# Kernel optimization log

Measured on AMD Instinct MI355X. Metric: run time of the kernel, lower is better.

## Reference

```python
import jax, jax.numpy as jnp
import numpy as np

N_HEADS = 8; DH = 64; G = 4; K = 9
C = N_HEADS * DH; CG = C // G
FACTOR = 2.0; TAU = 1.0
SCALE = DH ** -0.5


def _conv1x1(x, w, b):
    # x: (C, *spatial), w: (O, C), b: (O,)
    y = jnp.tensordot(w, x, axes=([1], [0]))
    return y + b.reshape((-1,) + (1,) * (y.ndim - 1))


def _dwconv(x, w, b):
    # depthwise 3x3, SAME padding; x (N,Cg,H,W), w (Cg,1,3,3)
    y = jax.lax.conv_general_dilated(x, w, (1, 1), 'SAME',
                                     feature_group_count=x.shape[1],
                                     dimension_numbers=('NCHW', 'OIHW', 'NCHW'))
    return y + b[None, :, None, None]


def _ln(x, g, b):
    # LayerNormProxy: LN over channel dim of NCHW (torch default eps=1e-5)
    m = jnp.mean(x, axis=1, keepdims=True)
    v = jnp.var(x, axis=1, keepdims=True)
    return (x - m) / jnp.sqrt(v + 1e-5) * g[None, :, None, None] + b[None, :, None, None]


def _grid_sample(img, grid):
    # bilinear, align_corners=True, padding_mode='zeros'
    # img (N,C,H,W), grid (N,Hg,Wg,2) with (x,y) in [-1,1]
    N, Cc, H, W = img.shape
    gx = (grid[..., 0] + 1.0) * 0.5 * (W - 1)
    gy = (grid[..., 1] + 1.0) * 0.5 * (H - 1)
    x0 = jnp.floor(gx); y0 = jnp.floor(gy)

    def g(yy, xx):
        yi = jnp.clip(yy, 0, H - 1).astype(jnp.int32)
        xi = jnp.clip(xx, 0, W - 1).astype(jnp.int32)
        ok = ((yy >= 0) & (yy <= H - 1) & (xx >= 0) & (xx <= W - 1)).astype(img.dtype)
        vals = jax.vmap(lambda im, a, b: im[:, a, b])(img, yi, xi)  # (N,C,Hg,Wg)
        return vals * ok[:, None]

    wx1 = gx - x0; wx0 = 1.0 - wx1
    wy1 = gy - y0; wy0 = 1.0 - wy1
    return (g(y0, x0) * (wy0 * wx0)[:, None]
            + g(y0, x0 + 1) * (wy0 * wx1)[:, None]
            + g(y0 + 1, x0) * (wy1 * wx0)[:, None]
            + g(y0 + 1, x0 + 1) * (wy1 * wx1)[:, None])


def _forward(x, idx, labels, wq, bq, wk, bk, wv, bv, wo, bo,
             ow1, ob1, g1, b1, ow2, ob2, g2, b2, ow3):
    _, _, H, W = x.shape
    n = idx.shape[0]
    iy, ix = idx[:, 0], idx[:, 1]

    q = _conv1x1(x[0], wq, bq)[None]               # (1,C,H,W)
    q_off = q.reshape(G, CG, H, W)                 # (b g) c h w with b=1
    q_sel = q[0][:, iy, ix]                        # (C,n)

    # offset predictor: dwconv -> LN -> GELU (x2) -> 1x1 (no bias)
    t = jax.nn.gelu(_ln(_dwconv(q_off, ow1, ob1), g1, b1), approximate=False)
    t = jax.nn.gelu(_ln(_dwconv(t, ow2, ob2), g2, b2), approximate=False)
    offset = jnp.einsum('gchw,oc->gohw', t, ow3)   # (G,2K,H,W)

    # offset_range_factor > 0: tanh * [1/H,1/W] (tiled K times) * factor
    rng = jnp.tile(jnp.array([1.0 / H, 1.0 / W], offset.dtype), K)
    offset = jnp.tanh(offset) * rng[None, :, None, None] * FACTOR
    off = offset.transpose(0, 2, 3, 1).reshape(G, H, W, K, 2)  # (g,h,w,K,(y,x))

    # reference points in [-1,1] (y,x), unfolded over 3x3 window w/ replication pad
    ry = (jnp.arange(H, dtype=x.dtype) + 0.5) / H * 2.0 - 1.0
    rx = (jnp.arange(W, dtype=x.dtype) + 0.5) / W * 2.0 - 1.0
    ref = jnp.stack(jnp.meshgrid(ry, rx, indexing='ij'), 0)    # (2,H,W)
    pad = jnp.pad(ref, ((0, 0), (1, 1), (1, 1)), mode='edge')
    patches = jnp.stack([pad[:, dy:dy + H, dx:dx + W]
                         for dy in range(3) for dx in range(3)], 0)  # (K,2,H,W)
    ref_unf = patches.transpose(2, 3, 0, 1)                    # (H,W,K,2)

    pos = off + ref_unf[None]                                  # (G,H,W,K,2)
    pos = pos.transpose(0, 3, 1, 2, 4).reshape(G * K, H, W, 2)
    grid = pos[..., ::-1]                                      # (x,y) order

    # gather per-group channels at K learned locations per position
    xg = x.reshape(G, CG, H, W)
    img = jnp.broadcast_to(xg[:, None], (G, K, CG, H, W)).reshape(G * K, CG, H, W)
    xs = _grid_sample(img, grid)                               # (GK,CG,H,W)
    xs = xs.reshape(G, K, CG, H, W).transpose(0, 2, 1, 3, 4).reshape(C, K, H, W)
    xs_sel = xs[:, :, iy, ix]                                  # (C,K,n)

    k = _conv1x1(xs_sel, wk, bk).reshape(N_HEADS, DH, K, n).transpose(0, 1, 3, 2)  # (h,d,n,K)
    v = _conv1x1(xs_sel, wv, bv).reshape(N_HEADS, DH, K, n).transpose(0, 1, 3, 2)
    qh = q_sel.reshape(N_HEADS, DH, n)

    attn = jnp.einsum('hdn,hdnk->hnk', qh, k) * SCALE
    attn = jax.nn.softmax(attn / TAU, axis=-1)                 # (h,n,K)
    out = jnp.einsum('hnk,hdnk->hdn', attn, v).reshape(C, n)
    y = _conv1x1(out, wo, bo).T                                # (n, dim_out)

    sig = jax.nn.sigmoid(y[jnp.arange(n), labels])

    # second grid_sample over full channels at the same learned positions
    img_full = jnp.broadcast_to(x, (G * K, C, H, W))
    xr = _grid_sample(img_full, grid)                          # (GK,C,H,W)
    xr_sel = xr[:, :, iy, ix].transpose(2, 0, 1)               # (n,GK,C)
    return y, attn, xr_sel, sig


def setup_inputs() -> dict:
    key = jax.random.key(0)
    ks = jax.random.split(key, 16)
    H = W = 64; n = 2048; s = 0.02
    return dict(
        x=jax.random.normal(ks[0], (1, C, H, W), jnp.float32),
        idx=jax.random.randint(ks[1], (n, 2), 0, H),
        labels=jax.random.randint(ks[2], (n,), 0, C),
        wq=jax.random.normal(ks[3], (C, C), jnp.float32) * s, bq=jnp.zeros((C,), jnp.float32),
        wk=jax.random.normal(ks[4], (C, C), jnp.float32) * s, bk=jnp.zeros((C,), jnp.float32),
        wv=jax.random.normal(ks[5], (C, C), jnp.float32) * s, bv=jnp.zeros((C,), jnp.float32),
        wo=jax.random.normal(ks[6], (C, C), jnp.float32) * s, bo=jnp.zeros((C,), jnp.float32),
        ow1=jax.random.normal(ks[7], (CG, 1, 3, 3), jnp.float32) * s, ob1=jnp.zeros((CG,), jnp.float32),
        g1=jnp.ones((CG,), jnp.float32), b1=jnp.zeros((CG,), jnp.float32),
        ow2=jax.random.normal(ks[8], (CG, 1, 3, 3), jnp.float32) * s, ob2=jnp.zeros((CG,), jnp.float32),
        g2=jnp.ones((CG,), jnp.float32), b2=jnp.zeros((CG,), jnp.float32),
        ow3=jax.random.normal(ks[9], (2 * K, CG), jnp.float32) * s,
    )


def reference(x, idx, labels, wq, bq, wk, bk, wv, bv, wo, bo,
              ow1, ob1, g1, b1, ow2, ob2, g2, b2, ow3):
    return _forward(x, idx, labels, wq, bq, wk, bk, wv, bv, wo, bo,
                    ow1, ob1, g1, b1, ow2, ob2, g2, b2, ow3)
```

## Files before the change

### kernel.cpp

```cpp
#include <hip/hip_runtime.h>
#include <math.h>

namespace {

typedef unsigned short u16;
typedef unsigned int u32;
typedef __attribute__((ext_vector_type(8))) short bf16x8;
typedef __attribute__((ext_vector_type(4))) float f32x4;
typedef __attribute__((ext_vector_type(2))) float f32x2;

constexpr int HDIM = 64;
constexpr int WDIM = 64;
constexpr int HW = HDIM * WDIM;
constexpr int C = 512;
constexpr int G = 4;
constexpr int CG = 128;
constexpr int K = 9;
constexpr int NH = 8;
constexpr float SCALE = 0.125f;

__device__ __forceinline__ u16 f2b(float f) {
  union { float f; u32 u; } v; v.f = f;
  u32 u = v.u;
  return (u16)((u + 0x7FFFu + ((u >> 16) & 1u)) >> 16);
}
__device__ __forceinline__ float b2f(u16 b) {
  union { u32 u; float f; } v; v.u = ((u32)b) << 16;
  return v.f;
}

__global__ void k_convert3(const float* __restrict__ a, const float* __restrict__ b,
                           const float* __restrict__ c, u16* __restrict__ da,
                           u16* __restrict__ db, u16* __restrict__ dc) {
  int j = blockIdx.x * 256 + threadIdx.x;
  da[j] = f2b(a[j]);
  db[j] = f2b(b[j]);
  dc[j] = f2b(c[j]);
}

__global__ void k_wkT(const float* __restrict__ wk, u16* __restrict__ wkT) {
  __shared__ float tile[32][33];
  int r0 = blockIdx.x * 32;
  int c0 = blockIdx.y * 32;
  int tx = threadIdx.x, ty = threadIdx.y;
  for (int r = ty; r < 32; r += 8)
    tile[r][tx] = wk[(r0 + r) * C + c0 + tx];
  __syncthreads();
  for (int r = ty; r < 32; r += 8)
    wkT[(c0 + r) * C + r0 + tx] = f2b(tile[tx][r]);
}

__global__ void k_transpose(const float* __restrict__ x, u16* __restrict__ xtb) {
  __shared__ float tile[32][33];
  int p0 = blockIdx.x * 32;
  int c0 = blockIdx.y * 32;
  int tx = threadIdx.x, ty = threadIdx.y;
  for (int r = ty; r < 32; r += 8)
    tile[r][tx] = x[(c0 + r) * HW + p0 + tx];
  __syncthreads();
  for (int r = ty; r < 32; r += 8)
    xtb[(p0 + r) * C + c0 + tx] = f2b(tile[tx][r]);
}

template <bool OUT_BF16>
__global__ void __launch_bounds__(256)
k_gemm_mfma(const u16* __restrict__ A, int lda, int aOffZ,
            const u16* __restrict__ BT, int ldb, int bOffZ,
            const float* __restrict__ bias, int biasOffZ,
            void* __restrict__ Dp, int ldd, int dOffZ, int Kd) {
  int z = blockIdx.z;
  const u16* Ab = A + (size_t)z * aOffZ;
  const u16* Bb = BT + (size_t)z * bOffZ;
  int t = threadIdx.x;
  int wave = t >> 6, lane = t & 63;
  int wm = (wave >> 1) * 32, wn = (wave & 1) * 32;
  int bm = blockIdx.x * 64 + wm;
  int bn = blockIdx.y * 64 + wn;
  int row = lane & 15, quad = lane >> 4;
  f32x4 acc[2][2] = {};
  for (int k0 = 0; k0 < Kd; k0 += 32) {
    bf16x8 a[2], b[2];
#pragma unroll
    for (int mt = 0; mt < 2; ++mt)
      a[mt] = *(const bf16x8*)&Ab[(size_t)(bm + mt * 16 + row) * lda + k0 + quad * 8];
#pragma unroll
    for (int nt = 0; nt < 2; ++nt)
      b[nt] = *(const bf16x8*)&Bb[(size_t)(bn + nt * 16 + row) * ldb + k0 + quad * 8];
#pragma unroll
    for (int mt = 0; mt < 2; ++mt)
#pragma unroll
      for (int nt = 0; nt < 2; ++nt)
        acc[mt][nt] = __builtin_amdgcn_mfma_f32_16x16x32_bf16(a[mt], b[nt], acc[mt][nt], 0, 0, 0);
  }
#pragma unroll
  for (int nt = 0; nt < 2; ++nt) {
    int cc = bn + nt * 16 + row;
    float bb = bias ? bias[(size_t)z * biasOffZ + cc] : 0.0f;
#pragma unroll
    for (int mt = 0; mt < 2; ++mt)
#pragma unroll
      for (int r = 0; r < 4; ++r) {
        int rr = bm + mt * 16 + quad * 4 + r;
        float v = acc[mt][nt][r] + bb;
        if (OUT_BF16)
          ((u16*)Dp)[(size_t)z * dOffZ + (size_t)rr * ldd + cc] = f2b(v);
        else
          ((float*)Dp)[(size_t)z * dOffZ + (size_t)rr * ldd + cc] = v;
      }
  }
}

__global__ void __launch_bounds__(512)
k_dwln2(const u16* __restrict__ in, const float* __restrict__ w9,
        const float* __restrict__ wb, const float* __restrict__ lng,
        const float* __restrict__ lnb, u16* __restrict__ outp) {
  int p = blockIdx.x;
  int h = p >> 6, w = p & 63;
  int t = threadIdx.x;
  int cg = t & 127;
  float acc = wb[cg];
#pragma unroll
  for (int dy = 0; dy < 3; ++dy) {
    int hh = h + dy - 1;
    if (hh < 0 || hh >= HDIM) continue;
#pragma unroll
    for (int dx = 0; dx < 3; ++dx) {
      int ww = w + dx - 1;
      if (ww < 0 || ww >= WDIM) continue;
      acc += w9[cg * 9 + dy * 3 + dx] * b2f(in[(hh * WDIM + ww) * C + t]);
    }
  }
  float s = acc, s2 = acc * acc;
#pragma unroll
  for (int o = 32; o > 0; o >>= 1) {
    s += __shfl_xor(s, o, 64);
    s2 += __shfl_xor(s2, o, 64);
  }
  __shared__ float red[8][2];
  int wv = t >> 6;
  if ((t & 63) == 0) { red[wv][0] = s; red[wv][1] = s2; }
  __syncthreads();
  float S = red[wv][0] + red[wv ^ 1][0];
  float S2 = red[wv][1] + red[wv ^ 1][1];
  float mean = S * (1.0f / 128.0f);
  float var = S2 * (1.0f / 128.0f) - mean * mean;
  float xn = (acc - mean) * rsqrtf(var + 1e-5f) * lng[cg] + lnb[cg];
  outp[(size_t)p * C + t] = f2b(0.5f * xn * (1.0f + erff(xn * 0.70710678f)));
}

__global__ void __launch_bounds__(128)
k_offsets2(const u16* __restrict__ t2, const float* __restrict__ ow3,
           const int* __restrict__ idx, float* __restrict__ pos) {
  int i = blockIdx.x;
  int t = threadIdx.x;
  int iy = idx[2 * i], ix = idx[2 * i + 1];
  int p = iy * WDIM + ix;
  __shared__ float tl[512];
  __shared__ float ov[72];
#pragma unroll
  for (int j = 0; j < 4; ++j) tl[t + 128 * j] = b2f(t2[(size_t)p * C + t + 128 * j]);
  __syncthreads();
  if (t < 72) {
    int g = t / 18, l = t % 18;
    float a = 0.0f;
#pragma unroll 4
    for (int j = 0; j < 128; ++j) a += ow3[l * CG + j] * tl[g * CG + j];
    ov[t] = a;
  }
  __syncthreads();
  if (t < 36) {
    int g = t / 9, l = t % 9;
    int dy = l / 3, dx = l % 3;
    int ryi = min(max(iy + dy - 1, 0), HDIM - 1);
    int rxi = min(max(ix + dx - 1, 0), WDIM - 1);
    float ry = (ryi + 0.5f) * (2.0f / HDIM) - 1.0f;
    float rx = (rxi + 0.5f) * (2.0f / WDIM) - 1.0f;
    float py = tanhf(ov[g * 18 + 2 * l]) * (2.0f / HDIM) + ry;
    float px = tanhf(ov[g * 18 + 2 * l + 1]) * (2.0f / WDIM) + rx;
    int o = ((i * G + g) * K + l) * 2;
    pos[o] = py;
    pos[o + 1] = px;
  }
}

__global__ void k_qsel2(const u16* __restrict__ q_tb, const int* __restrict__ idx,
                        u16* __restrict__ qselb) {
  int i = blockIdx.x;
  int t = threadIdx.x;
  int p = idx[2 * i] * WDIM + idx[2 * i + 1];
  ((u32*)qselb)[(size_t)i * 256 + t] = ((const u32*)q_tb)[(size_t)p * 256 + t];
}

struct Bilin {
  const u16 *r00, *r01, *r10, *r11;
  float w00, w01, w10, w11;
};
__device__ __forceinline__ Bilin bilin(const u16* xtb, float py, float px, int coff) {
  float gx = (px + 1.0f) * 0.5f * (WDIM - 1);
  float gy = (py + 1.0f) * 0.5f * (HDIM - 1);
  float x0f = floorf(gx), y0f = floorf(gy);
  float wx1 = gx - x0f, wx0 = 1.0f - wx1;
  float wy1 = gy - y0f, wy0 = 1.0f - wy1;
  int x0 = (int)x0f, y0 = (int)y0f;
  int x1 = x0 + 1, y1 = y0 + 1;
  bool vx0 = (x0 >= 0) && (x0 < WDIM);
  bool vx1 = (x1 >= 0) && (x1 < WDIM);
  bool vy0 = (y0 >= 0) && (y0 < HDIM);
  bool vy1 = (y1 >= 0) && (y1 < HDIM);
  Bilin bl;
  bl.w00 = (vy0 && vx0) ? wy0 * wx0 : 0.0f;
  bl.w01 = (vy0 && vx1) ? wy0 * wx1 : 0.0f;
  bl.w10 = (vy1 && vx0) ? wy1 * wx0 : 0.0f;
  bl.w11 = (vy1 && vx1) ? wy1 * wx1 : 0.0f;
  int x0c = min(max(x0, 0), WDIM - 1), x1c = min(max(x1, 0), WDIM - 1);
  int y0c = min(max(y0, 0), HDIM - 1), y1c = min(max(y1, 0), HDIM - 1);
  bl.r00 = xtb + (y0c * WDIM + x0c) * C + coff;
  bl.r01 = xtb + (y0c * WDIM + x1c) * C + coff;
  bl.r10 = xtb + (y1c * WDIM + x0c) * C + coff;
  bl.r11 = xtb + (y1c * WDIM + x1c) * C + coff;
  return bl;
}

__global__ void __launch_bounds__(256)
k_sample2(const u16* __restrict__ xtb, const float* __restrict__ pos,
          float* __restrict__ xr) {
  int i = blockIdx.x >> 2;
  int g = blockIdx.x & 3;
  int t = threadIdx.x;
  int c2 = t * 2;
#pragma unroll 1
  for (int kk = 0; kk < K; ++kk) {
    int o = ((i * G + g) * K + kk) * 2;
    Bilin bl = bilin(xtb, pos[o], pos[o + 1], 0);
    u32 a00 = *(const u32*)&bl.r00[c2];
    u32 a01 = *(const u32*)&bl.r01[c2];
    u32 a10 = *(const u32*)&bl.r10[c2];
    u32 a11 = *(const u32*)&bl.r11[c2];
    float v0 = bl.w00 * b2f((u16)a00) + bl.w01 * b2f((u16)a01) +
               bl.w10 * b2f((u16)a10) + bl.w11 * b2f((u16)a11);
    float v1 = bl.w00 * b2f((u16)(a00 >> 16)) + bl.w01 * b2f((u16)(a01 >> 16)) +
               bl.w10 * b2f((u16)(a10 >> 16)) + bl.w11 * b2f((u16)(a11 >> 16));
    f32x2 ov = {v0, v1};
    size_t rbase = ((size_t)i * (G * K) + g * K + kk) * C;
    __builtin_nontemporal_store(ov, (f32x2*)&xr[rbase + c2]);
  }
}

__global__ void __launch_bounds__(256)
k_attn2(const u16* __restrict__ qk2b, const u16* __restrict__ xtb,
        const float* __restrict__ pos, float* __restrict__ attn_out,
        u16* __restrict__ z2b, int n) {
  constexpr int LD = 520;
  int i = blockIdx.x;
  int t = threadIdx.x;
  __shared__ alignas(16) u16 qkl[16 * LD];
  __shared__ alignas(16) u16 xsl[16 * LD];
  __shared__ float posl[72];
  __shared__ float lg[NH][K];
  __shared__ float pr[NH][K];
  const u16* qsrc = qk2b + (size_t)i * (NH * C);
  for (int j = t; j < NH * C; j += 256) qkl[(j >> 9) * LD + (j & 511)] = qsrc[j];
  if (t < 72) posl[t] = pos[(size_t)i * 72 + t];
  __syncthreads();
  int wave = t >> 6, lane = t & 63;
  {
    int g = wave;
#pragma unroll 1
    for (int kk = 0; kk < K; ++kk) {
      Bilin bl = bilin(xtb, posl[(g * K + kk) * 2], posl[(g * K + kk) * 2 + 1], g * CG);
      int c2 = lane * 2;
      u32 a00 = *(const u32*)&bl.r00[c2];
      u32 a01 = *(const u32*)&bl.r01[c2];
      u32 a10 = *(const u32*)&bl.r10[c2];
      u32 a11 = *(const u32*)&bl.r11[c2];
      float v0 = bl.w00 * b2f((u16)a00) + bl.w01 * b2f((u16)a01) +
                 bl.w10 * b2f((u16)a10) + bl.w11 * b2f((u16)a11);
      float v1 = bl.w00 * b2f((u16)(a00 >> 16)) + bl.w01 * b2f((u16)(a01 >> 16)) +
                 bl.w10 * b2f((u16)(a10 >> 16)) + bl.w11 * b2f((u16)(a11 >> 16));
      *(u32*)&xsl[kk * LD + g * CG + c2] = ((u32)f2b(v1) << 16) | f2b(v0);
    }
  }
  __syncthreads();
  if (wave == 0) {
    int row = lane & 15, quad = lane >> 4;
    f32x4 acc = {};
#pragma unroll 4
    for (int k0 = 0; k0 < C; k0 += 32) {
      bf16x8 a = *(const bf16x8*)&qkl[row * LD + k0 + quad * 8];
      bf16x8 b = *(const bf16x8*)&xsl[row * LD + k0 + quad * 8];
      acc = __builtin_amdgcn_mfma_f32_16x16x32_bf16(a, b, acc, 0, 0, 0);
    }
    if (row < K && quad < 2) {
#pragma unroll
      for (int r = 0; r < 4; ++r) lg[quad * 4 + r][row] = acc[r] * SCALE;
    }
  }
  __syncthreads();
  if (t < NH) {
    float mx = -1e30f;
    for (int kk = 0; kk < K; ++kk) mx = fmaxf(mx, lg[t][kk]);
    float sm = 0.0f;
    float e[K];
    for (int kk = 0; kk < K; ++kk) { e[kk] = expf(lg[t][kk] - mx); sm += e[kk]; }
    float inv = 1.0f / sm;
    for (int kk = 0; kk < K; ++kk) {
      float p = e[kk] * inv;
      pr[t][kk] = p;
      attn_out[((size_t)t * n + i) * K + kk] = p;
    }
  }
  __syncthreads();
  for (int j = t; j < NH * C; j += 256) {
    int h = j >> 9;
    int cc = j & 511;
    float a = 0.0f;
#pragma unroll
    for (int kk = 0; kk < K; ++kk) a += pr[h][kk] * b2f(xsl[kk * LD + cc]);
    z2b[(size_t)i * (NH * C) + j] = f2b(a);
  }
}

__global__ void k_sig(const float* __restrict__ y, const int* __restrict__ labels,
                      float* __restrict__ sig, int n) {
  int i = blockIdx.x * 256 + threadIdx.x;
  if (i >= n) return;
  float v = y[(size_t)i * C + labels[i]];
  sig[i] = 1.0f / (1.0f + expf(-v));
}

}

extern "C" void kernel_launch(void* const* d_in, const int* in_sizes, int n_in,
                              void* d_out, int out_size, void* d_ws, size_t ws_size,
                              hipStream_t stream) {
  (void)n_in; (void)out_size; (void)ws_size;
  const float* x = (const float*)d_in[0];
  const int* idx = (const int*)d_in[1];
  const int* labels = (const int*)d_in[2];
  const float* wq = (const float*)d_in[3];
  const float* bq = (const float*)d_in[4];
  const float* wk = (const float*)d_in[5];
  const float* wv = (const float*)d_in[7];
  const float* bv = (const float*)d_in[8];
  const float* wo = (const float*)d_in[9];
  const float* bo = (const float*)d_in[10];
  const float* ow1 = (const float*)d_in[11];
  const float* ob1 = (const float*)d_in[12];
  const float* g1 = (const float*)d_in[13];
  const float* b1 = (const float*)d_in[14];
  const float* ow2 = (const float*)d_in[15];
  const float* ob2 = (const float*)d_in[16];
  const float* g2 = (const float*)d_in[17];
  const float* b2 = (const float*)d_in[18];
  const float* ow3 = (const float*)d_in[19];
  int n = in_sizes[1] / 2;

  unsigned char* wp = (unsigned char*)d_ws;
  auto alloc = [&](size_t bytes) {
    unsigned char* p = wp;
    wp += (bytes + 255) & ~(size_t)255;
    return p;
  };
  u16* xtb = (u16*)alloc((size_t)HW * C * 2);
  u16* wqb = (u16*)alloc((size_t)C * C * 2);
  u16* wvb = (u16*)alloc((size_t)C * C * 2);
  u16* wob = (u16*)alloc((size_t)C * C * 2);
  u16* wkT = (u16*)alloc((size_t)C * C * 2);
  u16* q_tb = (u16*)alloc((size_t)HW * C * 2);
  u16* t1b = (u16*)alloc((size_t)HW * C * 2);
  u16* t2b = (u16*)alloc((size_t)HW * C * 2);
  u16* qselb = (u16*)alloc((size_t)n * C * 2);
  u16* qk2b = (u16*)alloc((size_t)n * NH * C * 2);
  float* pos = (float*)alloc((size_t)n * G * K * 2 * 4);
  u16* z2b = (u16*)alloc((size_t)n * NH * C * 2);
  u16* outb = (u16*)alloc((size_t)n * C * 2);

  float* out_f = (float*)d_out;
  float* y_out = out_f;
  float* attn_out = y_out + (size_t)n * C;
  float* xr_out = attn_out + (size_t)NH * n * K;
  float* sig_out = xr_out + (size_t)n * G * K * C;

  k_convert3<<<dim3(C * C / 256), 256, 0, stream>>>(wq, wv, wo, wqb, wvb, wob);
  k_wkT<<<dim3(C / 32, C / 32), dim3(32, 8), 0, stream>>>(wk, wkT);
  k_transpose<<<dim3(HW / 32, C / 32), dim3(32, 8), 0, stream>>>(x, xtb);

  k_gemm_mfma<true><<<dim3(HW / 64, C / 64, 1), 256, 0, stream>>>(
      xtb, C, 0, wqb, C, 0, bq, 0, q_tb, C, 0, C);

  k_dwln2<<<dim3(HW), 512, 0, stream>>>(q_tb, ow1, ob1, g1, b1, t1b);
  k_dwln2<<<dim3(HW), 512, 0, stream>>>(t1b, ow2, ob2, g2, b2, t2b);
  k_offsets2<<<dim3(n), 128, 0, stream>>>(t2b, ow3, idx, pos);
  k_qsel2<<<dim3(n), 256, 0, stream>>>(q_tb, idx, qselb);

  k_gemm_mfma<true><<<dim3(n / 64, C / 64, NH), 256, 0, stream>>>(
      qselb, C, 64, wkT, C, 64, nullptr, 0, qk2b, NH * C, C, 64);

  k_sample2<<<dim3(n * G), 256, 0, stream>>>(xtb, pos, xr_out);
  k_attn2<<<dim3(n), 256, 0, stream>>>(qk2b, xtb, pos, attn_out, z2b, n);

  k_gemm_mfma<true><<<dim3(n / 64, 1, NH), 256, 0, stream>>>(
      z2b, NH * C, C, wvb, C, 64 * C, bv, 64, outb, C, 64, C);

  k_gemm_mfma<false><<<dim3(n / 64, C / 64, 1), 256, 0, stream>>>(
      outb, C, 0, wob, C, 0, bo, 0, y_out, C, 0, C);

  k_sig<<<dim3((n + 255) / 256), 256, 0, stream>>>(y_out, labels, sig_out, n);
}
```

Baseline: 344.3 us.

## Fuse prep kernels, gather, sampling and sigmoid into neighbouring kernels

Merges the three weight/input conversion kernels into a single launch. The query-row gather now happens inside the GEMM through an index array, and the standalone bilinear-sampling kernel is folded into the attention kernel, which writes xr and fills shared memory in one pass. The sigmoid-on-label step moves into the final GEMM epilogue. k_dwln2 now processes two channels per thread with 256 threads, so each 128-channel group fits in one wave and the shared-memory reduction and barrier go away. This cuts launch count and redundant gathers, but the attention kernel now does four times the sampling work per block.

New measurement: 328.9 us. 4.5% less time.

```diff
diff --git a/kernel.cpp b/kernel.cpp
--- a/kernel.cpp
+++ b/kernel.cpp
@@ -29,45 +29,46 @@
   return v.f;
 }
 
-__global__ void k_convert3(const float* __restrict__ a, const float* __restrict__ b,
-                           const float* __restrict__ c, u16* __restrict__ da,
-                           u16* __restrict__ db, u16* __restrict__ dc) {
-  int j = blockIdx.x * 256 + threadIdx.x;
-  da[j] = f2b(a[j]);
-  db[j] = f2b(b[j]);
-  dc[j] = f2b(c[j]);
-}
-
-__global__ void k_wkT(const float* __restrict__ wk, u16* __restrict__ wkT) {
+__global__ void __launch_bounds__(256)
+k_prep(const float* __restrict__ wq, const float* __restrict__ wv,
+       const float* __restrict__ wo, const float* __restrict__ wk,
+       const float* __restrict__ x,
+       u16* __restrict__ wqb, u16* __restrict__ wvb, u16* __restrict__ wob,
+       u16* __restrict__ wkT, u16* __restrict__ xtb) {
+  int b = blockIdx.x;
+  int t = threadIdx.x;
+  if (b < 1024) {
+    int j = b * 256 + t;
+    wqb[j] = f2b(wq[j]);
+    wvb[j] = f2b(wv[j]);
+    wob[j] = f2b(wo[j]);
+    return;
+  }
   __shared__ float tile[32][33];
-  int r0 = blockIdx.x * 32;
-  int c0 = blockIdx.y * 32;
-  int tx = threadIdx.x, ty = threadIdx.y;
-  for (int r = ty; r < 32; r += 8)
-    tile[r][tx] = wk[(r0 + r) * C + c0 + tx];
-  __syncthreads();
-  for (int r = ty; r < 32; r += 8)
-    wkT[(c0 + r) * C + r0 + tx] = f2b(tile[tx][r]);
-}
-
-__global__ void k_transpose(const float* __restrict__ x, u16* __restrict__ xtb) {
-  __shared__ float tile[32][33];
-  int p0 = blockIdx.x * 32;
-  int c0 = blockIdx.y * 32;
-  int tx = threadIdx.x, ty = threadIdx.y;
-  for (int r = ty; r < 32; r += 8)
-    tile[r][tx] = x[(c0 + r) * HW + p0 + tx];
-  __syncthreads();
-  for (int r = ty; r < 32; r += 8)
-    xtb[(p0 + r) * C + c0 + tx] = f2b(tile[tx][r]);
+  int tx = t & 31, ty = t >> 5;
+  if (b < 1280) {
+    int bb = b - 1024;
+    int r0 = (bb & 15) * 32, c0 = (bb >> 4) * 32;
+    for (int r = ty; r < 32; r += 8) tile[r][tx] = wk[(r0 + r) * C + c0 + tx];
+    __syncthreads();
+    for (int r = ty; r < 32; r += 8) wkT[(c0 + r) * C + r0 + tx] = f2b(tile[tx][r]);
+  } else {
+    int bb = b - 1280;
+    int p0 = (bb & 127) * 32, c0 = (bb >> 7) * 32;
+    for (int r = ty; r < 32; r += 8) tile[r][tx] = x[(c0 + r) * HW + p0 + tx];
+    __syncthreads();
+    for (int r = ty; r < 32; r += 8) xtb[(p0 + r) * C + c0 + tx] = f2b(tile[tx][r]);
+  }
 }
 
 template <bool OUT_BF16>
 __global__ void __launch_bounds__(256)
 k_gemm_mfma(const u16* __restrict__ A, int lda, int aOffZ,
+            const int* __restrict__ aIdx,
             const u16* __restrict__ BT, int ldb, int bOffZ,
             const float* __restrict__ bias, int biasOffZ,
-            void* __restrict__ Dp, int ldd, int dOffZ, int Kd) {
+            void* __restrict__ Dp, int ldd, int dOffZ, int Kd,
+            const int* __restrict__ labels, float* __restrict__ sigp) {
   int z = blockIdx.z;
   const u16* Ab = A + (size_t)z * aOffZ;
   const u16* Bb = BT + (size_t)z * bOffZ;
@@ -77,12 +78,18 @@
   int bm = blockIdx.x * 64 + wm;
   int bn = blockIdx.y * 64 + wn;
   int row = lane & 15, quad = lane >> 4;
+  size_t ar[2];
+#pragma unroll
+  for (int mt = 0; mt < 2; ++mt) {
+    int r = bm + mt * 16 + row;
+    ar[mt] = aIdx ? (size_t)(aIdx[2 * r] * WDIM + aIdx[2 * r + 1]) : (size_t)r;
+  }
   f32x4 acc[2][2] = {};
   for (int k0 = 0; k0 < Kd; k0 += 32) {
     bf16x8 a[2], b[2];
 #pragma unroll
     for (int mt = 0; mt < 2; ++mt)
-      a[mt] = *(const bf16x8*)&Ab[(size_t)(bm + mt * 16 + row) * lda + k0 + quad * 8];
+      a[mt] = *(const bf16x8*)&Ab[ar[mt] * lda + k0 + quad * 8];
 #pragma unroll
     for (int nt = 0; nt < 2; ++nt)
       b[nt] = *(const bf16x8*)&Bb[(size_t)(bn + nt * 16 + row) * ldb + k0 + quad * 8];
@@ -102,23 +109,26 @@
       for (int r = 0; r < 4; ++r) {
         int rr = bm + mt * 16 + quad * 4 + r;
         float v = acc[mt][nt][r] + bb;
-        if (OUT_BF16)
+        if (OUT_BF16) {
           ((u16*)Dp)[(size_t)z * dOffZ + (size_t)rr * ldd + cc] = f2b(v);
-        else
+        } else {
           ((float*)Dp)[(size_t)z * dOffZ + (size_t)rr * ldd + cc] = v;
+          if (labels && labels[rr] == cc) sigp[rr] = 1.0f / (1.0f + expf(-v));
+        }
       }
   }
 }
 
-__global__ void __launch_bounds__(512)
+__global__ void __launch_bounds__(256)
 k_dwln2(const u16* __restrict__ in, const float* __restrict__ w9,
         const float* __restrict__ wb, const float* __restrict__ lng,
         const float* __restrict__ lnb, u16* __restrict__ outp) {
   int p = blockIdx.x;
   int h = p >> 6, w = p & 63;
   int t = threadIdx.x;
-  int cg = t & 127;
-  float acc = wb[cg];
+  int c0 = t * 2;
+  int cg0 = c0 & 127, cg1 = cg0 + 1;
+  float a0 = wb[cg0], a1 = wb[cg1];
 #pragma unroll
   for (int dy = 0; dy < 3; ++dy) {
     int hh = h + dy - 1;
@@ -127,25 +137,27 @@
     for (int dx = 0; dx < 3; ++dx) {
       int ww = w + dx - 1;
       if (ww < 0 || ww >= WDIM) continue;
-      acc += w9[cg * 9 + dy * 3 + dx] * b2f(in[(hh * WDIM + ww) * C + t]);
-    }
-  }
-  float s = acc, s2 = acc * acc;
+      u32 pr2 = *(const u32*)&in[(hh * WDIM + ww) * C + c0];
+      float wt0 = w9[cg0 * 9 + dy * 3 + dx];
+      float wt1 = w9[cg1 * 9 + dy * 3 + dx];
+      a0 += wt0 * b2f((u16)pr2);
+      a1 += wt1 * b2f((u16)(pr2 >> 16));
+    }
+  }
+  float s = a0 + a1, s2 = a0 * a0 + a1 * a1;
 #pragma unroll
   for (int o = 32; o > 0; o >>= 1) {
     s += __shfl_xor(s, o, 64);
     s2 += __shfl_xor(s2, o, 64);
   }
-  __shared__ float red[8][2];
-  int wv = t >> 6;
-  if ((t & 63) == 0) { red[wv][0] = s; red[wv][1] = s2; }
-  __syncthreads();
-  float S = red[wv][0] + red[wv ^ 1][0];
-  float S2 = red[wv][1] + red[wv ^ 1][1];
-  float mean = S * (1.0f / 128.0f);
-  float var = S2 * (1.0f / 128.0f) - mean * mean;
-  float xn = (acc - mean) * rsqrtf(var + 1e-5f) * lng[cg] + lnb[cg];
-  outp[(size_t)p * C + t] = f2b(0.5f * xn * (1.0f + erff(xn * 0.70710678f)));
+  float mean = s * (1.0f / 128.0f);
+  float var = s2 * (1.0f / 128.0f) - mean * mean;
+  float rstd = rsqrtf(var + 1e-5f);
+  float xn0 = (a0 - mean) * rstd * lng[cg0] + lnb[cg0];
+  float xn1 = (a1 - mean) * rstd * lng[cg1] + lnb[cg1];
+  u16 o0 = f2b(0.5f * xn0 * (1.0f + erff(xn0 * 0.70710678f)));
+  u16 o1 = f2b(0.5f * xn1 * (1.0f + erff(xn1 * 0.70710678f)));
+  *(u32*)&outp[(size_t)p * C + c0] = ((u32)o1 << 16) | o0;
 }
 
 __global__ void __launch_bounds__(128)
@@ -183,105 +195,72 @@
   }
 }
 
-__global__ void k_qsel2(const u16* __restrict__ q_tb, const int* __restrict__ idx,
-                        u16* __restrict__ qselb) {
-  int i = blockIdx.x;
-  int t = threadIdx.x;
-  int p = idx[2 * i] * WDIM + idx[2 * i + 1];
-  ((u32*)qselb)[(size_t)i * 256 + t] = ((const u32*)q_tb)[(size_t)p * 256 + t];
-}
-
-struct Bilin {
-  const u16 *r00, *r01, *r10, *r11;
-  float w00, w01, w10, w11;
-};
-__device__ __forceinline__ Bilin bilin(const u16* xtb, float py, float px, int coff) {
-  float gx = (px + 1.0f) * 0.5f * (WDIM - 1);
-  float gy = (py + 1.0f) * 0.5f * (HDIM - 1);
-  float x0f = floorf(gx), y0f = floorf(gy);
-  float wx1 = gx - x0f, wx0 = 1.0f - wx1;
-  float wy1 = gy - y0f, wy0 = 1.0f - wy1;
-  int x0 = (int)x0f, y0 = (int)y0f;
-  int x1 = x0 + 1, y1 = y0 + 1;
-  bool vx0 = (x0 >= 0) && (x0 < WDIM);
-  bool vx1 = (x1 >= 0) && (x1 < WDIM);
-  bool vy0 = (y0 >= 0) && (y0 < HDIM);
-  bool vy1 = (y1 >= 0) && (y1 < HDIM);
-  Bilin bl;
-  bl.w00 = (vy0 && vx0) ? wy0 * wx0 : 0.0f;
-  bl.w01 = (vy0 && vx1) ? wy0 * wx1 : 0.0f;
-  bl.w10 = (vy1 && vx0) ? wy1 * wx0 : 0.0f;
-  bl.w11 = (vy1 && vx1) ? wy1 * wx1 : 0.0f;
-  int x0c = min(max(x0, 0), WDIM - 1), x1c = min(max(x1, 0), WDIM - 1);
-  int y0c = min(max(y0, 0), HDIM - 1), y1c = min(max(y1, 0), HDIM - 1);
-  bl.r00 = xtb + (y0c * WDIM + x0c) * C + coff;
-  bl.r01 = xtb + (y0c * WDIM + x1c) * C + coff;
-  bl.r10 = xtb + (y1c * WDIM + x0c) * C + coff;
-  bl.r11 = xtb + (y1c * WDIM + x1c) * C + coff;
-  return bl;
-}
-
 __global__ void __launch_bounds__(256)
-k_sample2(const u16* __restrict__ xtb, const float* __restrict__ pos,
-          float* __restrict__ xr) {
-  int i = blockIdx.x >> 2;
-  int g = blockIdx.x & 3;
-  int t = threadIdx.x;
-  int c2 = t * 2;
-#pragma unroll 1
-  for (int kk = 0; kk < K; ++kk) {
-    int o = ((i * G + g) * K + kk) * 2;
-    Bilin bl = bilin(xtb, pos[o], pos[o + 1], 0);
-    u32 a00 = *(const u32*)&bl.r00[c2];
-    u32 a01 = *(const u32*)&bl.r01[c2];
-    u32 a10 = *(const u32*)&bl.r10[c2];
-    u32 a11 = *(const u32*)&bl.r11[c2];
-    float v0 = bl.w00 * b2f((u16)a00) + bl.w01 * b2f((u16)a01) +
-               bl.w10 * b2f((u16)a10) + bl.w11 * b2f((u16)a11);
-    float v1 = bl.w00 * b2f((u16)(a00 >> 16)) + bl.w01 * b2f((u16)(a01 >> 16)) +
-               bl.w10 * b2f((u16)(a10 >> 16)) + bl.w11 * b2f((u16)(a11 >> 16));
-    f32x2 ov = {v0, v1};
-    size_t rbase = ((size_t)i * (G * K) + g * K + kk) * C;
-    __builtin_nontemporal_store(ov, (f32x2*)&xr[rbase + c2]);
-  }
-}
-
-__global__ void __launch_bounds__(256)
-k_attn2(const u16* __restrict__ qk2b, const u16* __restrict__ xtb,
+k_attn3(const u16* __restrict__ qk2b, const u16* __restrict__ xtb,
         const float* __restrict__ pos, float* __restrict__ attn_out,
-        u16* __restrict__ z2b, int n) {
+        u16* __restrict__ z2b, float* __restrict__ xr, int n) {
   constexpr int LD = 520;
   int i = blockIdx.x;
   int t = threadIdx.x;
   __shared__ alignas(16) u16 qkl[16 * LD];
   __shared__ alignas(16) u16 xsl[16 * LD];
-  __shared__ float posl[72];
+  __shared__ int ro[36][4];
+  __shared__ float wbl[36][4];
   __shared__ float lg[NH][K];
   __shared__ float pr[NH][K];
   const u16* qsrc = qk2b + (size_t)i * (NH * C);
   for (int j = t; j < NH * C; j += 256) qkl[(j >> 9) * LD + (j & 511)] = qsrc[j];
-  if (t < 72) posl[t] = pos[(size_t)i * 72 + t];
-  __syncthreads();
-  int wave = t >> 6, lane = t & 63;
-  {
-    int g = wave;
+  if (t < 36) {
+    float py = pos[(size_t)i * 72 + 2 * t];
+    float px = pos[(size_t)i * 72 + 2 * t + 1];
+    float gx = (px + 1.0f) * 0.5f * (WDIM - 1);
+    float gy = (py + 1.0f) * 0.5f * (HDIM - 1);
+    float x0f = floorf(gx), y0f = floorf(gy);
+    float wx1 = gx - x0f, wx0 = 1.0f - wx1;
+    float wy1 = gy - y0f, wy0 = 1.0f - wy1;
+    int x0 = (int)x0f, y0 = (int)y0f;
+    int x1 = x0 + 1, y1 = y0 + 1;
+    bool vx0 = (x0 >= 0) && (x0 < WDIM);
+    bool vx1 = (x1 >= 0) && (x1 < WDIM);
+    bool vy0 = (y0 >= 0) && (y0 < HDIM);
+    bool vy1 = (y1 >= 0) && (y1 < HDIM);
+    wbl[t][0] = (vy0 && vx0) ? wy0 * wx0 : 0.0f;
+    wbl[t][1] = (vy0 && vx1) ? wy0 * wx1 : 0.0f;
+    wbl[t][2] = (vy1 && vx0) ? wy1 * wx0 : 0.0f;
+    wbl[t][3] = (vy1 && vx1) ? wy1 * wx1 : 0.0f;
+    int x0c = min(max(x0, 0), WDIM - 1), x1c = min(max(x1, 0), WDIM - 1);
+    int y0c = min(max(y0, 0), HDIM - 1), y1c = min(max(y1, 0), HDIM - 1);
+    ro[t][0] = (y0c * WDIM + x0c) * C;
+    ro[t][1] = (y0c * WDIM + x1c) * C;
+    ro[t][2] = (y1c * WDIM + x0c) * C;
+    ro[t][3] = (y1c * WDIM + x1c) * C;
+  }
+  __syncthreads();
+  int wave = t >> 6;
+  int c2 = t * 2;
+  float* xrb = xr + (size_t)i * (G * K) * C;
+#pragma unroll 1
+  for (int g = 0; g < G; ++g) {
 #pragma unroll 1
     for (int kk = 0; kk < K; ++kk) {
-      Bilin bl = bilin(xtb, posl[(g * K + kk) * 2], posl[(g * K + kk) * 2 + 1], g * CG);
-      int c2 = lane * 2;
-      u32 a00 = *(const u32*)&bl.r00[c2];
-      u32 a01 = *(const u32*)&bl.r01[c2];
-      u32 a10 = *(const u32*)&bl.r10[c2];
-      u32 a11 = *(const u32*)&bl.r11[c2];
-      float v0 = bl.w00 * b2f((u16)a00) + bl.w01 * b2f((u16)a01) +
-                 bl.w10 * b2f((u16)a10) + bl.w11 * b2f((u16)a11);
-      float v1 = bl.w00 * b2f((u16)(a00 >> 16)) + bl.w01 * b2f((u16)(a01 >> 16)) +
-                 bl.w10 * b2f((u16)(a10 >> 16)) + bl.w11 * b2f((u16)(a11 >> 16));
-      *(u32*)&xsl[kk * LD + g * CG + c2] = ((u32)f2b(v1) << 16) | f2b(v0);
+      int it = g * K + kk;
+      float w00 = wbl[it][0], w01 = wbl[it][1], w10 = wbl[it][2], w11 = wbl[it][3];
+      u32 a00 = *(const u32*)&xtb[ro[it][0] + c2];
+      u32 a01 = *(const u32*)&xtb[ro[it][1] + c2];
+      u32 a10 = *(const u32*)&xtb[ro[it][2] + c2];
+      u32 a11 = *(const u32*)&xtb[ro[it][3] + c2];
+      float v0 = w00 * b2f((u16)a00) + w01 * b2f((u16)a01) +
+                 w10 * b2f((u16)a10) + w11 * b2f((u16)a11);
+      float v1 = w00 * b2f((u16)(a00 >> 16)) + w01 * b2f((u16)(a01 >> 16)) +
+                 w10 * b2f((u16)(a10 >> 16)) + w11 * b2f((u16)(a11 >> 16));
+      f32x2 ov = {v0, v1};
+      __builtin_nontemporal_store(ov, (f32x2*)&xrb[(size_t)it * C + c2]);
+      if (wave == g) *(u32*)&xsl[kk * LD + c2] = ((u32)f2b(v1) << 16) | f2b(v0);
     }
   }
   __syncthreads();
   if (wave == 0) {
+    int lane = t & 63;
     int row = lane & 15, quad = lane >> 4;
     f32x4 acc = {};
 #pragma unroll 4
@@ -318,14 +297,6 @@
     for (int kk = 0; kk < K; ++kk) a += pr[h][kk] * b2f(xsl[kk * LD + cc]);
     z2b[(size_t)i * (NH * C) + j] = f2b(a);
   }
-}
-
-__global__ void k_sig(const float* __restrict__ y, const int* __restrict__ labels,
-                      float* __restrict__ sig, int n) {
-  int i = blockIdx.x * 256 + threadIdx.x;
-  if (i >= n) return;
-  float v = y[(size_t)i * C + labels[i]];
-  sig[i] = 1.0f / (1.0f + expf(-v));
 }
 
 }
@@ -369,7 +340,6 @@
   u16* q_tb = (u16*)alloc((size_t)HW * C * 2);
   u16* t1b = (u16*)alloc((size_t)HW * C * 2);
   u16* t2b = (u16*)alloc((size_t)HW * C * 2);
-  u16* qselb = (u16*)alloc((size_t)n * C * 2);
   u16* qk2b = (u16*)alloc((size_t)n * NH * C * 2);
   float* pos = (float*)alloc((size_t)n * G * K * 2 * 4);
   u16* z2b = (u16*)alloc((size_t)n * NH * C * 2);
@@ -381,29 +351,23 @@
   float* xr_out = attn_out + (size_t)NH * n * K;
   float* sig_out = xr_out + (size_t)n * G * K * C;
 
-  k_convert3<<<dim3(C * C / 256), 256, 0, stream>>>(wq, wv, wo, wqb, wvb, wob);
-  k_wkT<<<dim3(C / 32, C / 32), dim3(32, 8), 0, stream>>>(wk, wkT);
-  k_transpose<<<dim3(HW / 32, C / 32), dim3(32, 8), 0, stream>>>(x, xtb);
+  k_prep<<<dim3(3328), 256, 0, stream>>>(wq, wv, wo, wk, x, wqb, wvb, wob, wkT, xtb);
 
   k_gemm_mfma<true><<<dim3(HW / 64, C / 64, 1), 256, 0, stream>>>(
-      xtb, C, 0, wqb, C, 0, bq, 0, q_tb, C, 0, C);
-
-  k_dwln2<<<dim3(HW), 512, 0, stream>>>(q_tb, ow1, ob1, g1, b1, t1b);
-  k_dwln2<<<dim3(HW), 512, 0, stream>>>(t1b, ow2, ob2, g2, b2, t2b);
+      xtb, C, 0, nullptr, wqb, C, 0, bq, 0, q_tb, C, 0, C, nullptr, nullptr);
+
+  k_dwln2<<<dim3(HW), 256, 0, stream>>>(q_tb, ow1, ob1, g1, b1, t1b);
+  k_dwln2<<<dim3(HW), 256, 0, stream>>>(t1b, ow2, ob2, g2, b2, t2b);
   k_offsets2<<<dim3(n), 128, 0, stream>>>(t2b, ow3, idx, pos);
-  k_qsel2<<<dim3(n), 256, 0, stream>>>(q_tb, idx, qselb);
 
   k_gemm_mfma<true><<<dim3(n / 64, C / 64, NH), 256, 0, stream>>>(
-      qselb, C, 64, wkT, C, 64, nullptr, 0, qk2b, NH * C, C, 64);
-
-  k_sample2<<<dim3(n * G), 256, 0, stream>>>(xtb, pos, xr_out);
-  k_attn2<<<dim3(n), 256, 0, stream>>>(qk2b, xtb, pos, attn_out, z2b, n);
+      q_tb, C, 64, idx, wkT, C, 64, nullptr, 0, qk2b, NH * C, C, 64, nullptr, nullptr);
+
+  k_attn3<<<dim3(n), 256, 0, stream>>>(qk2b, xtb, pos, attn_out, z2b, xr_out, n);
 
   k_gemm_mfma<true><<<dim3(n / 64, 1, NH), 256, 0, stream>>>(
-      z2b, NH * C, C, wvb, C, 64 * C, bv, 64, outb, C, 64, C);
+      z2b, NH * C, C, nullptr, wvb, C, 64 * C, bv, 64, outb, C, 64, C, nullptr, nullptr);
 
   k_gemm_mfma<false><<<dim3(n / 64, C / 64, 1), 256, 0, stream>>>(
-      outb, C, 0, wob, C, 0, bo, 0, y_out, C, 0, C);
-
-  k_sig<<<dim3((n + 255) / 256), 256, 0, stream>>>(y_out, labels, sig_out, n);
-}
+      outb, C, 0, nullptr, wob, C, 0, bo, 0, y_out, C, 0, C, labels, sig_out);
+}
```
